# Optimization experiments

Measured on AMD Instinct MI355X. Metric: run time of the kernel, lower is better.

The kernel has to match this reference:

```python
import jax, jax.numpy as jnp
import numpy as np

NEG_SLOPE = 0.2

def gat_conv(x, W, att_src, att_dst, src, dst, num_nodes, concat):
    # x: [N, F_in], W: [F_in, H*C], att_*: [H, C]
    H, C = att_src.shape
    h = (x @ W).reshape(-1, H, C)                      # [N, H, C]
    a_src = jnp.sum(h * att_src[None], axis=-1)        # [N, H]
    a_dst = jnp.sum(h * att_dst[None], axis=-1)        # [N, H]
    # per-edge raw attention: alpha_j (source) + alpha_i (target)
    alpha = a_src[src] + a_dst[dst]                    # [E, H]
    alpha = jax.nn.leaky_relu(alpha, NEG_SLOPE)
    # segment softmax over incoming edges of each destination node
    amax = jax.ops.segment_max(alpha, dst, num_segments=num_nodes)  # [N, H]
    amax = jnp.where(jnp.isfinite(amax), amax, 0.0)
    ex = jnp.exp(alpha - amax[dst])                    # [E, H]
    denom = jax.ops.segment_sum(ex, dst, num_segments=num_nodes)    # [N, H]
    attn = ex / (denom[dst] + 1e-16)                   # [E, H]
    # attention-weighted scatter-add aggregation
    msg = h[src] * attn[..., None]                     # [E, H, C]
    out = jax.ops.segment_sum(msg, dst, num_segments=num_nodes)     # [N, H, C]
    if concat:
        return out.reshape(num_nodes, H * C)
    return out.mean(axis=1)


def setup_inputs() -> dict:
    key = jax.random.key(0)
    ks = jax.random.split(key, 8)
    N, E = 100000, 1600000
    F_in, Hid, Hd, F_out = 256, 32, 8, 64
    glorot = lambda k, shape: jax.random.uniform(
        k, shape, jnp.float32, -1.0, 1.0) * jnp.sqrt(6.0 / (shape[0] + shape[-1]))
    x = jax.random.normal(ks[0], (N, F_in), jnp.float32)
    edge_index = jax.random.randint(ks[1], (2, E), 0, N, jnp.int64)
    W1 = glorot(ks[2], (F_in, Hd * Hid))
    att_src1 = glorot(ks[3], (Hd, Hid))
    att_dst1 = glorot(ks[4], (Hd, Hid))
    W2 = glorot(ks[5], (Hd * Hid, 1 * F_out))
    att_src2 = glorot(ks[6], (1, F_out))
    att_dst2 = glorot(ks[7], (1, F_out))
    return {"x": x, "W1": W1, "att_src1": att_src1, "att_dst1": att_dst1,
            "W2": W2, "att_src2": att_src2, "att_dst2": att_dst2,
            "edge_index": edge_index}


def reference(x, W1, att_src1, att_dst1, W2, att_src2, att_dst2, edge_index):
    src, dst = edge_index[0], edge_index[1]
    N = x.shape[0]
    # dropout is inactive in eval mode
    h = gat_conv(x, W1, att_src1, att_dst1, src, dst, N, concat=True)
    h = jax.nn.elu(h)
    out = gat_conv(h, W2, att_src2, att_dst2, src, dst, N, concat=False)
    return out
```

## Files before the change

### kernel.cpp

```cpp
#include <hip/hip_runtime.h>
#include <hip/hip_bf16.h>

#define LRELU(a) ((a) >= 0.0f ? (a) : 0.2f * (a))

typedef __attribute__((ext_vector_type(8))) _Float16 f16x8;
typedef __attribute__((ext_vector_type(4))) _Float16 f16x4;
typedef __attribute__((ext_vector_type(4))) float f32x4;

__global__ __launch_bounds__(256) void cvt_w_both(const float* __restrict__ W1,
                                                  const float* __restrict__ W2,
                                                  _Float16* __restrict__ T1,
                                                  _Float16* __restrict__ T2) {
    int t = blockIdx.x * 256 + threadIdx.x;
    if (t < 65536) {
        int k = t >> 8, n = t & 255;
        T1[n * 256 + k] = (_Float16)W1[t];
    } else {
        int u = t - 65536;
        if (u < 16384) {
            int k = u >> 6, n = u & 63;
            T2[n * 256 + k] = (_Float16)W2[u];
        }
    }
}

__global__ __launch_bounds__(512) void gemm1_mfma(
    const float* __restrict__ A,
    const _Float16* __restrict__ BT,
    const float* __restrict__ attS, const float* __restrict__ attD,
    _Float16* __restrict__ C, float* __restrict__ a_src, float* __restrict__ a_dst,
    int M) {
    const int K = 256;
    __shared__ _Float16 sA[128][40];
    __shared__ _Float16 sB[256][40];
    int tid = threadIdx.x;
    int m0 = blockIdx.y * 128;
    int wid = tid >> 6, lane = tid & 63;
    int wm = (wid >> 2) * 64, wn = (wid & 3) * 64;
    int lr = lane & 15, lg = lane >> 4;

    f32x4 acc[4][4];
    #pragma unroll
    for (int i = 0; i < 4; ++i)
        #pragma unroll
        for (int j = 0; j < 4; ++j)
            acc[i][j] = (f32x4){0.f, 0.f, 0.f, 0.f};

    for (int k0 = 0; k0 < K; k0 += 32) {
        {
            int row = tid >> 2, seg = tid & 3;
            int grow = m0 + row;
            float4 v0 = make_float4(0.f, 0.f, 0.f, 0.f), v1 = v0;
            if (grow < M) {
                v0 = *(const float4*)&A[(size_t)grow * K + k0 + seg * 8];
                v1 = *(const float4*)&A[(size_t)grow * K + k0 + seg * 8 + 4];
            }
            f16x8 hv;
            hv[0] = (_Float16)v0.x; hv[1] = (_Float16)v0.y;
            hv[2] = (_Float16)v0.z; hv[3] = (_Float16)v0.w;
            hv[4] = (_Float16)v1.x; hv[5] = (_Float16)v1.y;
            hv[6] = (_Float16)v1.z; hv[7] = (_Float16)v1.w;
            *(f16x8*)&sA[row][seg * 8] = hv;
        }
        #pragma unroll
        for (int rnd = 0; rnd < 2; ++rnd) {
            int idx = tid + rnd * 512;
            int row = idx >> 2, seg = idx & 3;
            *(f16x8*)&sB[row][seg * 8] = *(const f16x8*)&BT[(size_t)row * K + k0 + seg * 8];
        }
        __syncthreads();
        f16x8 bfr[4];
        #pragma unroll
        for (int i = 0; i < 4; ++i)
            bfr[i] = *(const f16x8*)&sB[wn + i * 16 + lr][lg * 8];
        #pragma unroll
        for (int mi = 0; mi < 4; ++mi) {
            f16x8 av = *(const f16x8*)&sA[wm + mi * 16 + lr][lg * 8];
            #pragma unroll
            for (int ni = 0; ni < 4; ++ni)
                acc[mi][ni] = __builtin_amdgcn_mfma_f32_16x16x32_f16(av, bfr[ni], acc[mi][ni], 0, 0, 0);
        }
        __syncthreads();
    }

    float asv[4], adv[4];
    #pragma unroll
    for (int ni = 0; ni < 4; ++ni) {
        int col = wn + ni * 16 + lr;
        asv[ni] = attS[col];
        adv[ni] = attD[col];
    }
    int head0 = wn >> 5;
    #pragma unroll
    for (int mi = 0; mi < 4; ++mi) {
        #pragma unroll
        for (int r = 0; r < 4; ++r) {
            int row = m0 + wm + mi * 16 + lg * 4 + r;
            float v0 = acc[mi][0][r], v1 = acc[mi][1][r];
            float v2 = acc[mi][2][r], v3 = acc[mi][3][r];
            float ps0 = v0 * asv[0] + v1 * asv[1], pd0 = v0 * adv[0] + v1 * adv[1];
            float ps1 = v2 * asv[2] + v3 * asv[3], pd1 = v2 * adv[2] + v3 * adv[3];
            #pragma unroll
            for (int msk = 8; msk >= 1; msk >>= 1) {
                ps0 += __shfl_xor(ps0, msk); pd0 += __shfl_xor(pd0, msk);
                ps1 += __shfl_xor(ps1, msk); pd1 += __shfl_xor(pd1, msk);
            }
            if (row < M) {
                C[(size_t)row * 256 + wn +  0 + lr] = (_Float16)v0;
                C[(size_t)row * 256 + wn + 16 + lr] = (_Float16)v1;
                C[(size_t)row * 256 + wn + 32 + lr] = (_Float16)v2;
                C[(size_t)row * 256 + wn + 48 + lr] = (_Float16)v3;
                if (lr == 0) {
                    a_src[(size_t)row * 8 + head0]     = ps0;
                    a_dst[(size_t)row * 8 + head0]     = pd0;
                    a_src[(size_t)row * 8 + head0 + 1] = ps1;
                    a_dst[(size_t)row * 8 + head0 + 1] = pd1;
                }
            }
        }
    }
}

__global__ __launch_bounds__(256) void gemm2_mfma(
    const _Float16* __restrict__ A,
    const _Float16* __restrict__ BT,
    const float* __restrict__ attS, const float* __restrict__ attD,
    _Float16* __restrict__ C, float* __restrict__ a_src, float* __restrict__ a_dst,
    int M) {
    const int K = 256;
    __shared__ _Float16 sA[128][40];
    __shared__ _Float16 sB[64][40];
    int tid = threadIdx.x;
    int m0 = blockIdx.y * 128;
    int wid = tid >> 6, lane = tid & 63;
    int wm = wid * 32;
    int lr = lane & 15, lg = lane >> 4;

    f32x4 acc[2][4];
    #pragma unroll
    for (int i = 0; i < 2; ++i)
        #pragma unroll
        for (int j = 0; j < 4; ++j)
            acc[i][j] = (f32x4){0.f, 0.f, 0.f, 0.f};

    for (int k0 = 0; k0 < K; k0 += 32) {
        #pragma unroll
        for (int rnd = 0; rnd < 2; ++rnd) {
            int idx = tid + rnd * 256;
            int row = idx >> 2, seg = idx & 3;
            int grow = m0 + row;
            f16x8 va = {0, 0, 0, 0, 0, 0, 0, 0};
            if (grow < M) va = *(const f16x8*)&A[(size_t)grow * K + k0 + seg * 8];
            *(f16x8*)&sA[row][seg * 8] = va;
        }
        {
            int row = tid >> 2, seg = tid & 3;
            *(f16x8*)&sB[row][seg * 8] = *(const f16x8*)&BT[(size_t)row * K + k0 + seg * 8];
        }
        __syncthreads();
        f16x8 bfr[4];
        #pragma unroll
        for (int i = 0; i < 4; ++i)
            bfr[i] = *(const f16x8*)&sB[i * 16 + lr][lg * 8];
        #pragma unroll
        for (int mi = 0; mi < 2; ++mi) {
            f16x8 av = *(const f16x8*)&sA[wm + mi * 16 + lr][lg * 8];
            #pragma unroll
            for (int ni = 0; ni < 4; ++ni)
                acc[mi][ni] = __builtin_amdgcn_mfma_f32_16x16x32_f16(av, bfr[ni], acc[mi][ni], 0, 0, 0);
        }
        __syncthreads();
    }

    float asv[4], adv[4];
    #pragma unroll
    for (int ni = 0; ni < 4; ++ni) {
        asv[ni] = attS[ni * 16 + lr];
        adv[ni] = attD[ni * 16 + lr];
    }
    #pragma unroll
    for (int mi = 0; mi < 2; ++mi) {
        #pragma unroll
        for (int r = 0; r < 4; ++r) {
            int row = m0 + wm + mi * 16 + lg * 4 + r;
            float ps = 0.f, pd = 0.f;
            #pragma unroll
            for (int ni = 0; ni < 4; ++ni) {
                float v = acc[mi][ni][r];
                ps += v * asv[ni];
                pd += v * adv[ni];
            }
            #pragma unroll
            for (int msk = 8; msk >= 1; msk >>= 1) {
                ps += __shfl_xor(ps, msk);
                pd += __shfl_xor(pd, msk);
            }
            if (row < M) {
                #pragma unroll
                for (int ni = 0; ni < 4; ++ni)
                    C[(size_t)row * 64 + ni * 16 + lr] = (_Float16)acc[mi][ni][r];
                if (lr == 0) { a_src[row] = ps; a_dst[row] = pd; }
            }
        }
    }
}

__global__ __launch_bounds__(256) void hist_dst(const int* __restrict__ dst, unsigned* __restrict__ cnt,
                                                int* __restrict__ pos, int E) {
    int e = blockIdx.x * 256 + threadIdx.x;
    if (e < E) pos[e] = (int)atomicAdd(&cnt[dst[e]], 1u);
}

__global__ __launch_bounds__(256) void scan_partial(const unsigned* __restrict__ cnt,
                                                    int* __restrict__ rowptr,
                                                    unsigned* __restrict__ bsum, int n) {
    __shared__ unsigned s[256];
    int i = blockIdx.x * 256 + threadIdx.x;
    unsigned v = (i < n) ? cnt[i] : 0u;
    s[threadIdx.x] = v;
    __syncthreads();
    #pragma unroll
    for (int off = 1; off < 256; off <<= 1) {
        unsigned t = (threadIdx.x >= off) ? s[threadIdx.x - off] : 0u;
        __syncthreads();
        s[threadIdx.x] += t;
        __syncthreads();
    }
    if (i < n) rowptr[i + 1] = (int)s[threadIdx.x];
    if (threadIdx.x == 255) bsum[blockIdx.x] = s[255];
}

__global__ __launch_bounds__(512) void scan_bsum(unsigned* __restrict__ bsum, int nb) {
    __shared__ unsigned s[512];
    int t = threadIdx.x;
    s[t] = (t < nb) ? bsum[t] : 0u;
    __syncthreads();
    #pragma unroll
    for (int off = 1; off < 512; off <<= 1) {
        unsigned v = (t >= off) ? s[t - off] : 0u;
        __syncthreads();
        s[t] += v;
        __syncthreads();
    }
    unsigned ex = (t == 0) ? 0u : s[t - 1];
    if (t < nb) bsum[t] = ex;
}

__global__ __launch_bounds__(256) void scan_add(int* __restrict__ rowptr, const unsigned* __restrict__ boff, int n) {
    int i = blockIdx.x * 256 + threadIdx.x;
    if (i < n) rowptr[i + 1] += (int)boff[blockIdx.x];
    if (blockIdx.x == 0 && threadIdx.x == 0) rowptr[0] = 0;
}

__global__ __launch_bounds__(256) void scatter_srcs(const int* __restrict__ src, const int* __restrict__ dst,
                                                    const int* __restrict__ rowptr, const int* __restrict__ pos,
                                                    int* __restrict__ srcs, int E) {
    int e = blockIdx.x * 256 + threadIdx.x;
    if (e >= E) return;
    srcs[rowptr[dst[e]] + pos[e]] = src[e];
}

__global__ __launch_bounds__(256) void agg1(const int* __restrict__ srcs,
                                            const int* __restrict__ begA,
                                            const int* __restrict__ endB,
                                            const float* __restrict__ a_src,
                                            const float* __restrict__ a_dst,
                                            const _Float16* __restrict__ h1,
                                            _Float16* __restrict__ o1, int N) {
    int wid = threadIdx.x >> 6;
    int lane = threadIdx.x & 63;
    int d = blockIdx.x * 4 + wid;
    if (d >= N) return;
    int beg = begA[d], end = endB[d];
    int e8 = lane & 7;
    int hd = lane >> 3;
    float adst = a_dst[(size_t)d * 8 + hd];
    const char* h1b = (const char*)h1;
    const char* asb = (const char*)a_src;
    unsigned loff = (unsigned)(lane << 3);

    float4 acc = make_float4(0.f, 0.f, 0.f, 0.f);
    float wsum = 0.0f;
    for (int j0 = beg; j0 < end; j0 += 8) {
        int nb = end - j0;
        int s2 = 0; float w = 0.f;
        if (e8 < nb) {
            s2 = srcs[j0 + e8];
            float a = *(const float*)(asb + (((unsigned)s2 << 5) + ((unsigned)hd << 2))) + adst;
            a = LRELU(a);
            w = __expf(a);
        }
        wsum += w;
        if (nb >= 8) {
            float at[8]; unsigned sb[8];
            #pragma unroll
            for (int t = 0; t < 8; ++t) {
                int sl = (lane & 56) | t;
                at[t] = __shfl(w, sl);
                sb[t] = ((unsigned)__shfl(s2, sl)) << 9;
            }
            f16x4 hv[8];
            #pragma unroll
            for (int t = 0; t < 8; ++t)
                hv[t] = *(const f16x4*)(h1b + (sb[t] + loff));
            #pragma unroll
            for (int t = 0; t < 8; ++t) {
                acc.x += (float)hv[t][0] * at[t];
                acc.y += (float)hv[t][1] * at[t];
                acc.z += (float)hv[t][2] * at[t];
                acc.w += (float)hv[t][3] * at[t];
            }
        } else {
            for (int t = 0; t < nb; ++t) {
                int sl = (lane & 56) | t;
                float at = __shfl(w, sl);
                int s = __shfl(s2, sl);
                f16x4 hq = *(const f16x4*)(h1b + (((unsigned)s << 9) + loff));
                acc.x += (float)hq[0] * at;
                acc.y += (float)hq[1] * at;
                acc.z += (float)hq[2] * at;
                acc.w += (float)hq[3] * at;
            }
        }
    }
    wsum += __shfl_xor(wsum, 1);
    wsum += __shfl_xor(wsum, 2);
    wsum += __shfl_xor(wsum, 4);
    float rw = 1.0f / (wsum + 1e-16f);
    acc.x *= rw; acc.y *= rw; acc.z *= rw; acc.w *= rw;
    acc.x = acc.x > 0.0f ? acc.x : expm1f(acc.x);
    acc.y = acc.y > 0.0f ? acc.y : expm1f(acc.y);
    acc.z = acc.z > 0.0f ? acc.z : expm1f(acc.z);
    acc.w = acc.w > 0.0f ? acc.w : expm1f(acc.w);
    f16x4 hh;
    hh[0] = (_Float16)acc.x;
    hh[1] = (_Float16)acc.y;
    hh[2] = (_Float16)acc.z;
    hh[3] = (_Float16)acc.w;
    *(f16x4*)(o1 + (size_t)d * 256 + lane * 4) = hh;
}

__global__ __launch_bounds__(256) void agg2(const int* __restrict__ srcs,
                                            const int* __restrict__ begA,
                                            const int* __restrict__ endB,
                                            const float* __restrict__ a_src,
                                            const float* __restrict__ a_dst,
                                            const _Float16* __restrict__ h2,
                                            float* __restrict__ out, int N) {
    int wid = threadIdx.x >> 6;
    int lane = threadIdx.x & 63;
    int d = blockIdx.x * 4 + wid;
    if (d >= N) return;
    int beg = begA[d], end = endB[d];
    float adst = a_dst[d];
    const char* h2b = (const char*)h2;
    int grp = lane >> 4;
    int cid = lane & 15;

    float4 acc = make_float4(0.f, 0.f, 0.f, 0.f);
    float wsum = 0.0f;
    for (int j0 = beg; j0 < end; j0 += 64) {
        int nb = end - j0; if (nb > 64) nb = 64;
        int s2 = 0; float w = 0.f;
        if (lane < nb) {
            s2 = srcs[j0 + lane];
            float a = LRELU(a_src[s2] + adst);
            w = __expf(a);
        }
        wsum += w;
        int tmax = (nb + 3) >> 2;
        for (int t = 0; t < tmax; ++t) {
            int ei = 4 * t + grp;
            float at = __shfl(w, ei);
            int s = __shfl(s2, ei);
            f16x4 hv = *(const f16x4*)(h2b + (((unsigned)s << 7) + ((unsigned)cid << 3)));
            acc.x += (float)hv[0] * at;
            acc.y += (float)hv[1] * at;
            acc.z += (float)hv[2] * at;
            acc.w += (float)hv[3] * at;
        }
    }
    #pragma unroll
    for (int mask = 16; mask <= 32; mask <<= 1) {
        acc.x += __shfl_xor(acc.x, mask);
        acc.y += __shfl_xor(acc.y, mask);
        acc.z += __shfl_xor(acc.z, mask);
        acc.w += __shfl_xor(acc.w, mask);
    }
    #pragma unroll
    for (int mask = 1; mask < 64; mask <<= 1)
        wsum += __shfl_xor(wsum, mask);
    float rw = 1.0f / (wsum + 1e-16f);
    if (lane < 16) {
        float4 o = make_float4(acc.x * rw, acc.y * rw, acc.z * rw, acc.w * rw);
        *(float4*)(out + (size_t)d * 64 + cid * 4) = o;
    }
}

extern "C" void kernel_launch(void* const* d_in, const int* in_sizes, int n_in,
                              void* d_out, int out_size, void* d_ws, size_t ws_size,
                              hipStream_t stream) {
    const float* x        = (const float*)d_in[0];
    const float* W1       = (const float*)d_in[1];
    const float* att_src1 = (const float*)d_in[2];
    const float* att_dst1 = (const float*)d_in[3];
    const float* W2       = (const float*)d_in[4];
    const float* att_src2 = (const float*)d_in[5];
    const float* att_dst2 = (const float*)d_in[6];
    const int*   ei       = (const int*)d_in[7];

    int N = in_sizes[0] / 256;
    int E = in_sizes[7] / 2;
    const int* src = ei;
    const int* dst = ei + E;

    _Float16* out1 = (_Float16*)d_ws;
    _Float16* h1f  = out1 + (size_t)N * 256;
    float* a_src1v = (float*)(h1f + (size_t)N * 256);
    float* a_dst1v = a_src1v + (size_t)N * 8;
    float* a_src2v = a_dst1v + (size_t)N * 8;
    float* a_dst2v = a_src2v + N;
    int*   rowptr  = (int*)(a_dst2v + N);
    unsigned* cnt  = (unsigned*)(rowptr + N + 1);
    unsigned* bsum = cnt + N;
    int*   pos     = (int*)(bsum + 512);
    int*   srcs    = pos + E;
    _Float16* w1t  = (_Float16*)(srcs + E);
    _Float16* w2t  = w1t + 65536;

    _Float16* h2f = h1f;

    float* outf = (float*)d_out;
    int nb = (N + 255) / 256;

    hipMemsetAsync(cnt, 0, (size_t)N * sizeof(unsigned), stream);
    hist_dst<<<(E + 255) / 256, 256, 0, stream>>>(dst, cnt, pos, E);
    scan_partial<<<nb, 256, 0, stream>>>(cnt, rowptr, bsum, N);
    scan_bsum<<<1, 512, 0, stream>>>(bsum, nb);
    scan_add<<<nb, 256, 0, stream>>>(rowptr, bsum, N);
    scatter_srcs<<<(E + 255) / 256, 256, 0, stream>>>(src, dst, rowptr, pos, srcs, E);

    cvt_w_both<<<(65536 + 16384 + 255) / 256, 256, 0, stream>>>(W1, W2, w1t, w2t);

    gemm1_mfma<<<dim3(1, (N + 127) / 128), 512, 0, stream>>>(x, w1t,
                                                             att_src1, att_dst1,
                                                             h1f, a_src1v, a_dst1v, N);
    agg1<<<(N + 3) / 4, 256, 0, stream>>>(srcs, rowptr, rowptr + 1, a_src1v, a_dst1v, h1f, out1, N);

    gemm2_mfma<<<dim3(1, (N + 127) / 128), 256, 0, stream>>>(out1, w2t,
                                                             att_src2, att_dst2,
                                                             h2f, a_src2v, a_dst2v, N);
    agg2<<<(N + 3) / 4, 256, 0, stream>>>(srcs, rowptr, rowptr + 1, a_src2v, a_dst2v, h2f, outf, N);
}
```

Before: 390.7 us.

## Prefetch GEMM tiles into registers and batch gather loads in aggregation kernels

```diff
diff --git a/kernel.cpp b/kernel.cpp
--- a/kernel.cpp
+++ b/kernel.cpp
@@ -31,14 +31,22 @@
     _Float16* __restrict__ C, float* __restrict__ a_src, float* __restrict__ a_dst,
     int M) {
     const int K = 256;
-    __shared__ _Float16 sA[128][40];
-    __shared__ _Float16 sB[256][40];
+    __shared__ _Float16 sAs[128][40];
+    __shared__ _Float16 sBs[256][40];
     int tid = threadIdx.x;
     int m0 = blockIdx.y * 128;
     int wid = tid >> 6, lane = tid & 63;
     int wm = (wid >> 2) * 64, wn = (wid & 3) * 64;
     int lr = lane & 15, lg = lane >> 4;
 
+    int rA = tid >> 2, sA8 = (tid & 3) * 8;
+    int growA = m0 + rA;
+    bool mok = growA < M;
+    const float* Ap = A + (size_t)growA * K + sA8;
+    int rB0 = tid >> 2, rB1 = rB0 + 128, sB8 = (tid & 3) * 8;
+    const _Float16* Bp0 = BT + (size_t)rB0 * K + sB8;
+    const _Float16* Bp1 = BT + (size_t)rB1 * K + sB8;
+
     f32x4 acc[4][4];
     #pragma unroll
     for (int i = 0; i < 4; ++i)
@@ -46,36 +54,43 @@
         for (int j = 0; j < 4; ++j)
             acc[i][j] = (f32x4){0.f, 0.f, 0.f, 0.f};
 
+    float4 pa0 = make_float4(0.f, 0.f, 0.f, 0.f), pa1 = pa0;
+    f16x8 pb0, pb1;
+    if (mok) {
+        pa0 = *(const float4*)(Ap + 0);
+        pa1 = *(const float4*)(Ap + 4);
+    }
+    pb0 = *(const f16x8*)Bp0;
+    pb1 = *(const f16x8*)Bp1;
+
     for (int k0 = 0; k0 < K; k0 += 32) {
         {
-            int row = tid >> 2, seg = tid & 3;
-            int grow = m0 + row;
-            float4 v0 = make_float4(0.f, 0.f, 0.f, 0.f), v1 = v0;
-            if (grow < M) {
-                v0 = *(const float4*)&A[(size_t)grow * K + k0 + seg * 8];
-                v1 = *(const float4*)&A[(size_t)grow * K + k0 + seg * 8 + 4];
-            }
             f16x8 hv;
-            hv[0] = (_Float16)v0.x; hv[1] = (_Float16)v0.y;
-            hv[2] = (_Float16)v0.z; hv[3] = (_Float16)v0.w;
-            hv[4] = (_Float16)v1.x; hv[5] = (_Float16)v1.y;
-            hv[6] = (_Float16)v1.z; hv[7] = (_Float16)v1.w;
-            *(f16x8*)&sA[row][seg * 8] = hv;
-        }
-        #pragma unroll
-        for (int rnd = 0; rnd < 2; ++rnd) {
-            int idx = tid + rnd * 512;
-            int row = idx >> 2, seg = idx & 3;
-            *(f16x8*)&sB[row][seg * 8] = *(const f16x8*)&BT[(size_t)row * K + k0 + seg * 8];
-        }
-        __syncthreads();
+            hv[0] = (_Float16)pa0.x; hv[1] = (_Float16)pa0.y;
+            hv[2] = (_Float16)pa0.z; hv[3] = (_Float16)pa0.w;
+            hv[4] = (_Float16)pa1.x; hv[5] = (_Float16)pa1.y;
+            hv[6] = (_Float16)pa1.z; hv[7] = (_Float16)pa1.w;
+            *(f16x8*)&sAs[rA][sA8] = hv;
+            *(f16x8*)&sBs[rB0][sB8] = pb0;
+            *(f16x8*)&sBs[rB1][sB8] = pb1;
+        }
+        __syncthreads();
+        if (k0 + 32 < K) {
+            int ko = k0 + 32;
+            if (mok) {
+                pa0 = *(const float4*)(Ap + ko + 0);
+                pa1 = *(const float4*)(Ap + ko + 4);
+            }
+            pb0 = *(const f16x8*)(Bp0 + ko);
+            pb1 = *(const f16x8*)(Bp1 + ko);
+        }
         f16x8 bfr[4];
         #pragma unroll
         for (int i = 0; i < 4; ++i)
-            bfr[i] = *(const f16x8*)&sB[wn + i * 16 + lr][lg * 8];
+            bfr[i] = *(const f16x8*)&sBs[wn + i * 16 + lr][lg * 8];
         #pragma unroll
         for (int mi = 0; mi < 4; ++mi) {
-            f16x8 av = *(const f16x8*)&sA[wm + mi * 16 + lr][lg * 8];
+            f16x8 av = *(const f16x8*)&sAs[wm + mi * 16 + lr][lg * 8];
             #pragma unroll
             for (int ni = 0; ni < 4; ++ni)
                 acc[mi][ni] = __builtin_amdgcn_mfma_f32_16x16x32_f16(av, bfr[ni], acc[mi][ni], 0, 0, 0);
@@ -128,14 +143,20 @@
     _Float16* __restrict__ C, float* __restrict__ a_src, float* __restrict__ a_dst,
     int M) {
     const int K = 256;
-    __shared__ _Float16 sA[128][40];
-    __shared__ _Float16 sB[64][40];
+    __shared__ _Float16 sAs[128][40];
+    __shared__ _Float16 sBs[64][40];
     int tid = threadIdx.x;
     int m0 = blockIdx.y * 128;
     int wid = tid >> 6, lane = tid & 63;
     int wm = wid * 32;
     int lr = lane & 15, lg = lane >> 4;
 
+    int rA0 = tid >> 2, rA1 = rA0 + 64, seg8 = (tid & 3) * 8;
+    bool mok0 = m0 + rA0 < M, mok1 = m0 + rA1 < M;
+    const _Float16* Ap0 = A + (size_t)(m0 + rA0) * K + seg8;
+    const _Float16* Ap1 = A + (size_t)(m0 + rA1) * K + seg8;
+    const _Float16* Bp = BT + (size_t)(tid >> 2) * K + seg8;
+
     f32x4 acc[2][4];
     #pragma unroll
     for (int i = 0; i < 2; ++i)
@@ -143,28 +164,29 @@
         for (int j = 0; j < 4; ++j)
             acc[i][j] = (f32x4){0.f, 0.f, 0.f, 0.f};
 
+    f16x8 pa0 = {0,0,0,0,0,0,0,0}, pa1 = pa0, pb;
+    if (mok0) pa0 = *(const f16x8*)Ap0;
+    if (mok1) pa1 = *(const f16x8*)Ap1;
+    pb = *(const f16x8*)Bp;
+
     for (int k0 = 0; k0 < K; k0 += 32) {
-        #pragma unroll
-        for (int rnd = 0; rnd < 2; ++rnd) {
-            int idx = tid + rnd * 256;
-            int row = idx >> 2, seg = idx & 3;
-            int grow = m0 + row;
-            f16x8 va = {0, 0, 0, 0, 0, 0, 0, 0};
-            if (grow < M) va = *(const f16x8*)&A[(size_t)grow * K + k0 + seg * 8];
-            *(f16x8*)&sA[row][seg * 8] = va;
-        }
-        {
-            int row = tid >> 2, seg = tid & 3;
-            *(f16x8*)&sB[row][seg * 8] = *(const f16x8*)&BT[(size_t)row * K + k0 + seg * 8];
-        }
-        __syncthreads();
+        *(f16x8*)&sAs[rA0][seg8] = pa0;
+        *(f16x8*)&sAs[rA1][seg8] = pa1;
+        *(f16x8*)&sBs[tid >> 2][seg8] = pb;
+        __syncthreads();
+        if (k0 + 32 < K) {
+            int ko = k0 + 32;
+            if (mok0) pa0 = *(const f16x8*)(Ap0 + ko);
+            if (mok1) pa1 = *(const f16x8*)(Ap1 + ko);
+            pb = *(const f16x8*)(Bp + ko);
+        }
         f16x8 bfr[4];
         #pragma unroll
         for (int i = 0; i < 4; ++i)
-            bfr[i] = *(const f16x8*)&sB[i * 16 + lr][lg * 8];
+            bfr[i] = *(const f16x8*)&sBs[i * 16 + lr][lg * 8];
         #pragma unroll
         for (int mi = 0; mi < 2; ++mi) {
-            f16x8 av = *(const f16x8*)&sA[wm + mi * 16 + lr][lg * 8];
+            f16x8 av = *(const f16x8*)&sAs[wm + mi * 16 + lr][lg * 8];
             #pragma unroll
             for (int ni = 0; ni < 4; ++ni)
                 acc[mi][ni] = __builtin_amdgcn_mfma_f32_16x16x32_f16(av, bfr[ni], acc[mi][ni], 0, 0, 0);
@@ -274,6 +296,7 @@
     int beg = begA[d], end = endB[d];
     int e8 = lane & 7;
     int hd = lane >> 3;
+    int base = lane & 56;
     float adst = a_dst[(size_t)d * 8 + hd];
     const char* h1b = (const char*)h1;
     const char* asb = (const char*)a_src;
@@ -281,41 +304,55 @@
 
     float4 acc = make_float4(0.f, 0.f, 0.f, 0.f);
     float wsum = 0.0f;
-    for (int j0 = beg; j0 < end; j0 += 8) {
+    for (int j0 = beg; j0 < end; j0 += 16) {
         int nb = end - j0;
-        int s2 = 0; float w = 0.f;
+        int sa = 0, sc = 0; float wa = 0.f, wb = 0.f;
         if (e8 < nb) {
-            s2 = srcs[j0 + e8];
-            float a = *(const float*)(asb + (((unsigned)s2 << 5) + ((unsigned)hd << 2))) + adst;
-            a = LRELU(a);
-            w = __expf(a);
-        }
-        wsum += w;
-        if (nb >= 8) {
-            float at[8]; unsigned sb[8];
+            sa = srcs[j0 + e8];
+            float a = *(const float*)(asb + (((unsigned)sa << 5) + ((unsigned)hd << 2))) + adst;
+            wa = __expf(LRELU(a));
+        }
+        if (e8 + 8 < nb) {
+            sc = srcs[j0 + e8 + 8];
+            float a = *(const float*)(asb + (((unsigned)sc << 5) + ((unsigned)hd << 2))) + adst;
+            wb = __expf(LRELU(a));
+        }
+        wsum += wa + wb;
+        if (nb >= 16) {
+            float at[16]; unsigned sb[16];
             #pragma unroll
             for (int t = 0; t < 8; ++t) {
-                int sl = (lane & 56) | t;
-                at[t] = __shfl(w, sl);
-                sb[t] = ((unsigned)__shfl(s2, sl)) << 9;
-            }
-            f16x4 hv[8];
-            #pragma unroll
-            for (int t = 0; t < 8; ++t)
+                at[t]     = __shfl(wa, base | t);
+                sb[t]     = ((unsigned)__shfl(sa, base | t)) << 9;
+                at[8 + t] = __shfl(wb, base | t);
+                sb[8 + t] = ((unsigned)__shfl(sc, base | t)) << 9;
+            }
+            f16x4 hv[16];
+            #pragma unroll
+            for (int t = 0; t < 16; ++t)
                 hv[t] = *(const f16x4*)(h1b + (sb[t] + loff));
             #pragma unroll
-            for (int t = 0; t < 8; ++t) {
+            for (int t = 0; t < 16; ++t) {
                 acc.x += (float)hv[t][0] * at[t];
                 acc.y += (float)hv[t][1] * at[t];
                 acc.z += (float)hv[t][2] * at[t];
                 acc.w += (float)hv[t][3] * at[t];
             }
         } else {
-            for (int t = 0; t < nb; ++t) {
-                int sl = (lane & 56) | t;
-                float at = __shfl(w, sl);
-                int s = __shfl(s2, sl);
-                f16x4 hq = *(const f16x4*)(h1b + (((unsigned)s << 9) + loff));
+            int n1 = nb < 8 ? nb : 8;
+            for (int t = 0; t < n1; ++t) {
+                float at = __shfl(wa, base | t);
+                unsigned sb = ((unsigned)__shfl(sa, base | t)) << 9;
+                f16x4 hq = *(const f16x4*)(h1b + (sb + loff));
+                acc.x += (float)hq[0] * at;
+                acc.y += (float)hq[1] * at;
+                acc.z += (float)hq[2] * at;
+                acc.w += (float)hq[3] * at;
+            }
+            for (int t = 8; t < nb; ++t) {
+                float at = __shfl(wb, base | (t - 8));
+                unsigned sb = ((unsigned)__shfl(sc, base | (t - 8))) << 9;
+                f16x4 hq = *(const f16x4*)(h1b + (sb + loff));
                 acc.x += (float)hq[0] * at;
                 acc.y += (float)hq[1] * at;
                 acc.z += (float)hq[2] * at;
@@ -356,6 +393,7 @@
     const char* h2b = (const char*)h2;
     int grp = lane >> 4;
     int cid = lane & 15;
+    unsigned coff = (unsigned)(cid << 3);
 
     float4 acc = make_float4(0.f, 0.f, 0.f, 0.f);
     float wsum = 0.0f;
@@ -369,15 +407,27 @@
         }
         wsum += w;
         int tmax = (nb + 3) >> 2;
-        for (int t = 0; t < tmax; ++t) {
-            int ei = 4 * t + grp;
-            float at = __shfl(w, ei);
-            int s = __shfl(s2, ei);
-            f16x4 hv = *(const f16x4*)(h2b + (((unsigned)s << 7) + ((unsigned)cid << 3)));
-            acc.x += (float)hv[0] * at;
-            acc.y += (float)hv[1] * at;
-            acc.z += (float)hv[2] * at;
-            acc.w += (float)hv[3] * at;
+        float at[16]; unsigned sb[16];
+        #pragma unroll
+        for (int t = 0; t < 16; ++t) {
+            if (t < tmax) {
+                int ei = 4 * t + grp;
+                at[t] = __shfl(w, ei);
+                sb[t] = ((unsigned)__shfl(s2, ei)) << 7;
+            }
+        }
+        f16x4 hv[16];
+        #pragma unroll
+        for (int t = 0; t < 16; ++t)
+            if (t < tmax) hv[t] = *(const f16x4*)(h2b + (sb[t] + coff));
+        #pragma unroll
+        for (int t = 0; t < 16; ++t) {
+            if (t < tmax) {
+                acc.x += (float)hv[t][0] * at[t];
+                acc.y += (float)hv[t][1] * at[t];
+                acc.z += (float)hv[t][2] * at[t];
+                acc.w += (float)hv[t][3] * at[t];
+            }
         }
     }
     #pragma unroll
```

Result: slower. 449.5 us (+15.0%).
